# Performance work log

Measured on AMD Instinct MI355X. Metric: run time of the kernel, lower is better.

Reference implementation:

```python
import jax, jax.numpy as jnp
import numpy as np

N_NODES = 50000
N_EDGES = 800000
NODE = 64
EDGE = 32
READOUT = 256
DEPTH = 4
NUM_GRAPHS = 512
BN_EPS = 1e-5

# Assumption (ffn / hidden_xavier_bn not in source): ffn = Linear + ReLU;
# hidden_xavier_bn = Linear -> BatchNorm (batch stats) -> ReLU.

def _ffn(h, W, b):
    return jax.nn.relu(h @ W + b)

def setup_inputs() -> dict:
    key = jax.random.key(0)
    ks = jax.random.split(key, 16)
    def lin(k, fin, fout):
        return jax.random.normal(k, (fin, fout), jnp.float32) / np.sqrt(fin)
    inp = {
        "x": jax.random.normal(ks[0], (N_NODES, NODE), jnp.float32),
        "edge_index": jax.random.randint(ks[1], (2, N_EDGES), 0, N_NODES),
        "edge_attr": jax.random.normal(ks[2], (N_EDGES, EDGE), jnp.float32),
        "w_atoms": jax.random.uniform(ks[3], (N_NODES,), jnp.float32),
        "w_bonds": jax.random.uniform(ks[4], (N_EDGES,), jnp.float32),
        "batch": jnp.sort(jax.random.randint(ks[5], (N_NODES,), 0, NUM_GRAPHS)),
        "V_W": lin(ks[6], NODE, NODE), "V_b": jnp.zeros((NODE,), jnp.float32),
        "E_W": lin(ks[7], EDGE, EDGE), "E_b": jnp.zeros((EDGE,), jnp.float32),
        "U_W": lin(ks[8], 2 * NODE + EDGE, NODE), "U_b": jnp.zeros((NODE,), jnp.float32),
        "R_W": lin(ks[9], NODE, READOUT), "R_b": jnp.zeros((READOUT,), jnp.float32),
        "R_gamma": jnp.ones((READOUT,), jnp.float32),
        "R_beta": jnp.zeros((READOUT,), jnp.float32),
    }
    return inp


def reference(x, edge_index, edge_attr, w_atoms, w_bonds, batch,
              V_W, V_b, E_W, E_b, U_W, U_b, R_W, R_b, R_gamma, R_beta):
    src, dst = edge_index[0], edge_index[1]  # x_j = x[src], aggregate at dst
    x_clone = x  # .clone().detach()

    # Edge FFN output is loop-invariant (same edge_attr each depth)
    m_ij = _ffn(edge_attr, E_W, E_b)  # [E, EDGE]

    def mp(h):
        m_j = _ffn(h[src], V_W, V_b)                              # [E, NODE]
        msg = w_bonds[:, None] * jnp.concatenate([m_j, m_ij], 1)  # [E, NODE+EDGE]
        aggr = jax.ops.segment_sum(msg, dst, num_segments=N_NODES)
        up = jax.nn.elu(jnp.concatenate([aggr, h], 1))            # [N, 2*NODE+EDGE]
        return _ffn(up, U_W, U_b) * w_atoms[:, None]              # [N, NODE]

    h = x
    last_x = None
    last_last_x = None
    for i in range(DEPTH):
        if i == 0 or i == 1:
            h = mp(h)
        else:
            h = mp(last_last_x + h)
        if i > 0:
            last_last_x = last_x
        last_x = h

    # Readout: Linear -> BatchNorm(batch stats) -> ReLU
    y = (h + x_clone) @ R_W + R_b
    mu = jnp.mean(y, axis=0)
    var = jnp.var(y, axis=0)
    y = jax.nn.relu((y - mu) * jax.lax.rsqrt(var + BN_EPS) * R_gamma + R_beta)

    # normalize_embedding=True -> scatter_mean over graphs
    sums = jax.ops.segment_sum(y, batch, num_segments=NUM_GRAPHS)
    cnts = jax.ops.segment_sum(jnp.ones((N_NODES,), y.dtype), batch,
                               num_segments=NUM_GRAPHS)
    return sums / jnp.maximum(cnts, 1.0)[:, None]
```

## Files before the change

### kernel.cpp

```cpp
#include <hip/hip_runtime.h>
#include <hip/hip_fp16.h>
#include <cstdint>
#include <cstddef>

#define NODE 64
#define EDGEF 32
#define UPF 160
#define RD 256
#define UT_STRIDE 162

typedef unsigned int uint4n __attribute__((ext_vector_type(4)));

__device__ __forceinline__ float eluf(float x) { return x > 0.f ? x : expm1f(x); }

union U32H2 { unsigned int u; __half2 h; };
union H16U { __half h; unsigned short u; };

__device__ __forceinline__ float2 h2f(unsigned int u) {
    U32H2 t; t.u = u;
    return __half22float2(t.h);
}
__device__ __forceinline__ unsigned short f2h(float f) {
    H16U t; t.h = __float2half_rn(f);
    return t.u;
}

__global__ void k_count(const int* __restrict__ dst, int* cnt, int* rank, int E) {
    int e = blockIdx.x * 256 + threadIdx.x;
    if (e < E) rank[e] = atomicAdd(&cnt[dst[e]], 1);
}

__global__ void k_scanA(const int* __restrict__ cnt, int* starts, int* bsum, int N) {
    __shared__ int sh[256];
    int t = threadIdx.x;
    int base = blockIdx.x * 1024 + t * 4;
    int v0 = 0, v1 = 0, v2 = 0, v3 = 0;
    if (base + 0 < N) v0 = cnt[base + 0];
    if (base + 1 < N) v1 = cnt[base + 1];
    if (base + 2 < N) v2 = cnt[base + 2];
    if (base + 3 < N) v3 = cnt[base + 3];
    int tot = v0 + v1 + v2 + v3;
    sh[t] = tot;
    __syncthreads();
    for (int off = 1; off < 256; off <<= 1) {
        int add = (t >= off) ? sh[t - off] : 0;
        __syncthreads();
        sh[t] += add;
        __syncthreads();
    }
    int excl = sh[t] - tot;
    if (base + 0 < N) starts[base + 0] = excl;
    if (base + 1 < N) starts[base + 1] = excl + v0;
    if (base + 2 < N) starts[base + 2] = excl + v0 + v1;
    if (base + 3 < N) starts[base + 3] = excl + v0 + v1 + v2;
    if (t == 255) bsum[blockIdx.x] = sh[255];
}

__global__ void k_scanB(const int* __restrict__ bsum, int* boff, int nb, int* starts, int N) {
    if (threadIdx.x == 0 && blockIdx.x == 0) {
        int run = 0;
        for (int b = 0; b < nb; ++b) { boff[b] = run; run += bsum[b]; }
        starts[N] = run;
    }
}

__global__ void k_scanC(const int* __restrict__ boff, int* starts, int N) {
    int i = blockIdx.x * 256 + threadIdx.x;
    if (i < N) starts[i] += boff[i >> 10];
}

__global__ void k_fill_ids(const int* __restrict__ src, const int* __restrict__ dst,
                           const float* __restrict__ wb, const int* __restrict__ rank,
                           const int* __restrict__ starts, uint4n* __restrict__ ecsr, int E) {
    int e = blockIdx.x * 256 + threadIdx.x;
    if (e >= E) return;
    int pos = starts[dst[e]] + rank[e];
    uint4n rec;
    rec.x = (unsigned int)src[e];
    rec.y = __float_as_uint(wb[e]);
    rec.z = (unsigned int)e;
    rec.w = 0u;
    __builtin_nontemporal_store(rec, &ecsr[pos]);
}

__global__ __launch_bounds__(256) void k_medge(
    const float* __restrict__ ea, const float* __restrict__ wb,
    const float* __restrict__ EW, const float* __restrict__ Eb,
    unsigned short* __restrict__ medge, int E) {
    __shared__ float ew_s[EDGEF * EDGEF];
    __shared__ float eb_s[EDGEF];
    int tid = threadIdx.x;
    for (int i = tid; i < EDGEF * EDGEF; i += 256) ew_s[i] = EW[i];
    if (tid < EDGEF) eb_s[tid] = Eb[tid];
    __syncthreads();
    int lane = tid & 63, wid = tid >> 6;
    int grp = lane >> 3, gl = lane & 7;
    const float4* ea4 = (const float4*)ea;
    float4 eb4 = *(const float4*)&eb_s[gl * 4];
    for (int e0 = blockIdx.x * 32; e0 < E; e0 += gridDim.x * 32) {
        int e = e0 + wid * 8 + grp;
        float4 a4 = {0.f, 0.f, 0.f, 0.f};
        float w = 0.f;
        if (e < E) {
            a4 = ea4[(size_t)e * 8 + gl];
            w = wb[e];
        }
        float4 m = eb4;
#pragma unroll
        for (int k = 0; k < EDGEF; ++k) {
            float av;
            switch (k & 3) {
                case 0: av = a4.x; break;
                case 1: av = a4.y; break;
                case 2: av = a4.z; break;
                default: av = a4.w; break;
            }
            float ak = __shfl(av, (lane & 56) | (k >> 2), 64);
            float4 w4 = *(const float4*)&ew_s[k * EDGEF + gl * 4];
            m.x = fmaf(ak, w4.x, m.x);
            m.y = fmaf(ak, w4.y, m.y);
            m.z = fmaf(ak, w4.z, m.z);
            m.w = fmaf(ak, w4.w, m.w);
        }
        if (e < E) {
            uint2 o;
            o.x = (unsigned int)f2h(w * fmaxf(m.x, 0.f)) |
                  ((unsigned int)f2h(w * fmaxf(m.y, 0.f)) << 16);
            o.y = (unsigned int)f2h(w * fmaxf(m.z, 0.f)) |
                  ((unsigned int)f2h(w * fmaxf(m.w, 0.f)) << 16);
            *(uint2*)(medge + (size_t)e * EDGEF + gl * 4) = o;
        }
    }
}

__global__ __launch_bounds__(256) void k_sumE(
    const unsigned short* __restrict__ medge, const uint4n* __restrict__ ecsr,
    const int* __restrict__ starts, float* __restrict__ aggrE_elu, int N) {
    int tid = threadIdx.x;
    int lane = tid & 63, wid = tid >> 6;
    int grp = lane >> 2, gl = lane & 3;
    int nwaves = gridDim.x * 4;
    for (int n = blockIdx.x * 4 + wid; n < N; n += nwaves) {
        int s0 = starts[n], s1 = starts[n + 1];
        float acc[8] = {0.f, 0.f, 0.f, 0.f, 0.f, 0.f, 0.f, 0.f};
        int i = s0 + grp;
        uint4 r0 = {0u,0u,0u,0u}, r1 = {0u,0u,0u,0u};
        if (i < s1)      r0 = *(const uint4*)(medge + (size_t)ecsr[i].z      * EDGEF + gl * 8);
        if (i + 16 < s1) r1 = *(const uint4*)(medge + (size_t)ecsr[i + 16].z * EDGEF + gl * 8);
        for (; i < s1; i += 16) {
            uint4 rN = {0u,0u,0u,0u};
            if (i + 32 < s1) rN = *(const uint4*)(medge + (size_t)ecsr[i + 32].z * EDGEF + gl * 8);
            float2 f0 = h2f(r0.x), f1 = h2f(r0.y), f2 = h2f(r0.z), f3 = h2f(r0.w);
            acc[0] += f0.x; acc[1] += f0.y;
            acc[2] += f1.x; acc[3] += f1.y;
            acc[4] += f2.x; acc[5] += f2.y;
            acc[6] += f3.x; acc[7] += f3.y;
            r0 = r1; r1 = rN;
        }
#pragma unroll
        for (int m2 = 4; m2 <= 32; m2 <<= 1) {
#pragma unroll
            for (int j = 0; j < 8; ++j) acc[j] += __shfl_xor(acc[j], m2, 64);
        }
        if (lane < 4) {
            float4 o0 = { eluf(acc[0]), eluf(acc[1]), eluf(acc[2]), eluf(acc[3]) };
            float4 o1 = { eluf(acc[4]), eluf(acc[5]), eluf(acc[6]), eluf(acc[7]) };
            float4* op = (float4*)(aggrE_elu + (size_t)n * EDGEF + gl * 8);
            op[0] = o0;
            op[1] = o1;
        }
    }
}

__global__ __launch_bounds__(256) void k_hv(
    const float* __restrict__ ha, const float* __restrict__ hb, int addB,
    const float* __restrict__ VW, const float* __restrict__ Vb,
    unsigned short* __restrict__ hvh, int N, int chunk) {
    __shared__ float slot[4][NODE];
    int tid = threadIdx.x;
    int lane = tid & 63, w = tid >> 6;
    float vcol[NODE];
#pragma unroll
    for (int k = 0; k < NODE; ++k) vcol[k] = VW[k * NODE + lane];
    float vb = Vb[lane];
    const float4* s4 = (const float4*)slot[w];
    int n0 = blockIdx.x * chunk;
    int n1 = n0 + chunk; if (n1 > N) n1 = N;
    for (int n = n0 + w; n < n1; n += 4) {
        float hrow = ha[(size_t)n * NODE + lane];
        if (addB) hrow += hb[(size_t)n * NODE + lane];
        slot[w][lane] = hrow;
        float d0 = 0.f, d1 = 0.f, d2 = 0.f, d3 = 0.f;
#pragma unroll
        for (int q = 0; q < 16; ++q) {
            float4 h4 = s4[q];
            d0 = fmaf(h4.x, vcol[4*q+0], d0);
            d1 = fmaf(h4.y, vcol[4*q+1], d1);
            d2 = fmaf(h4.z, vcol[4*q+2], d2);
            d3 = fmaf(h4.w, vcol[4*q+3], d3);
        }
        hvh[(size_t)n * NODE + lane] = f2h(fmaxf(vb + ((d0 + d1) + (d2 + d3)), 0.f));
    }
}

__global__ __launch_bounds__(512, 8) void k_gather(
    const unsigned short* __restrict__ hvh, const int* __restrict__ starts,
    const uint4n* __restrict__ ecsr, float* __restrict__ aggr, int N) {
    int lane = threadIdx.x & 63, wid = threadIdx.x >> 6;
    int grp = lane >> 3, gl = lane & 7;
    int nwaves = gridDim.x * 8;
    for (int n = blockIdx.x * 8 + wid; n < N; n += nwaves) {
        int s0 = starts[n], s1 = starts[n + 1];
        int deg = s1 - s0;
        float acc[8] = {0.f, 0.f, 0.f, 0.f, 0.f, 0.f, 0.f, 0.f};
        uint4 r0 = {0u,0u,0u,0u}, r1 = {0u,0u,0u,0u};
        float w0 = 0.f, w1 = 0.f;
        if (grp < deg) {
            uint4n c = ecsr[s0 + grp];
            r0 = *(const uint4*)(hvh + (size_t)c.x * NODE + gl * 8);
            w0 = __uint_as_float(c.y);
        }
        if (grp + 8 < deg) {
            uint4n c = ecsr[s0 + grp + 8];
            r1 = *(const uint4*)(hvh + (size_t)c.x * NODE + gl * 8);
            w1 = __uint_as_float(c.y);
        }
        for (int i = grp; i < deg; i += 8) {
            uint4 rN = {0u,0u,0u,0u}; float wN = 0.f;
            if (i + 16 < deg) {
                uint4n c = ecsr[s0 + i + 16];
                rN = *(const uint4*)(hvh + (size_t)c.x * NODE + gl * 8);
                wN = __uint_as_float(c.y);
            }
            float2 f0 = h2f(r0.x), f1 = h2f(r0.y), f2 = h2f(r0.z), f3 = h2f(r0.w);
            acc[0] = fmaf(w0, f0.x, acc[0]);
            acc[1] = fmaf(w0, f0.y, acc[1]);
            acc[2] = fmaf(w0, f1.x, acc[2]);
            acc[3] = fmaf(w0, f1.y, acc[3]);
            acc[4] = fmaf(w0, f2.x, acc[4]);
            acc[5] = fmaf(w0, f2.y, acc[5]);
            acc[6] = fmaf(w0, f3.x, acc[6]);
            acc[7] = fmaf(w0, f3.y, acc[7]);
            r0 = r1; w0 = w1;
            r1 = rN; w1 = wN;
        }
#pragma unroll
        for (int m2 = 8; m2 <= 32; m2 <<= 1) {
#pragma unroll
            for (int j = 0; j < 8; ++j) acc[j] += __shfl_xor(acc[j], m2, 64);
        }
        if (lane < 8) {
            float4* op = (float4*)(aggr + (size_t)n * NODE + gl * 8);
            float4 o0 = { acc[0], acc[1], acc[2], acc[3] };
            float4 o1 = { acc[4], acc[5], acc[6], acc[7] };
            op[0] = o0;
            op[1] = o1;
        }
    }
}

__global__ __launch_bounds__(512, 4) void k_update(
    const float* __restrict__ ha, const float* __restrict__ hb, int addB,
    const float* __restrict__ aggr, const float* __restrict__ aggrE_elu,
    const float* __restrict__ UW, const float* __restrict__ Ub,
    const float* __restrict__ watoms, float* __restrict__ h_out, int N) {
    __shared__ float lds_Ut[NODE * UT_STRIDE];
    __shared__ float lds_up[8 * UPF];
    int tid = threadIdx.x;
    for (int idx = tid; idx < UPF * NODE; idx += 512) {
        int j = idx & 63, t2 = idx >> 6;
        lds_Ut[j * UT_STRIDE + t2] = UW[idx];
    }
    int lane = tid & 63, wid = tid >> 6;
    float ub = Ub[lane];
    __syncthreads();
    float* myup = lds_up + wid * UPF;
    int nwaves = gridDim.x * 8;
    for (int n = blockIdx.x * 8 + wid; n < N; n += nwaves) {
        myup[lane] = eluf(aggr[(size_t)n * NODE + lane]);
        if (lane < EDGEF) myup[NODE + lane] = aggrE_elu[(size_t)n * EDGEF + lane];
        float hrow = ha[(size_t)n * NODE + lane];
        if (addB) hrow += hb[(size_t)n * NODE + lane];
        myup[NODE + EDGEF + lane] = eluf(hrow);
        float o = ub;
#pragma unroll
        for (int t2 = 0; t2 < UPF; t2 += 2) {
            float2 u2 = *(const float2*)&myup[t2];
            float2 w2 = *(const float2*)&lds_Ut[lane * UT_STRIDE + t2];
            o = fmaf(u2.x, w2.x, o);
            o = fmaf(u2.y, w2.y, o);
        }
        h_out[(size_t)n * NODE + lane] = fmaxf(o, 0.f) * watoms[n];
    }
}

__global__ __launch_bounds__(256) void k_y(
    const float* __restrict__ ha, const float* __restrict__ hb,
    const float* __restrict__ RW, const float* __restrict__ Rb,
    float* __restrict__ y, float* colsum, float* colsumsq, int N, int chunk) {
    __shared__ float slot[4][NODE];
    int tid = threadIdx.x;
    int lane = tid & 63, w = tid >> 6;
    float rcol[NODE];
#pragma unroll
    for (int k = 0; k < NODE; ++k) rcol[k] = RW[k * RD + w * 64 + lane];
    float rb = Rb[w * 64 + lane];
    const float4* s4 = (const float4*)slot[w];
    float sum = 0.f, sq = 0.f;
    int n0 = blockIdx.x * chunk;
    int n1 = n0 + chunk; if (n1 > N) n1 = N;
    for (int n = n0; n < n1; ++n) {
        float hvC = ha[(size_t)n * NODE + lane] + hb[(size_t)n * NODE + lane];
        slot[w][lane] = hvC;
        float d0 = 0.f, d1 = 0.f, d2 = 0.f, d3 = 0.f;
#pragma unroll
        for (int q = 0; q < 16; ++q) {
            float4 h4 = s4[q];
            d0 = fmaf(h4.x, rcol[4*q+0], d0);
            d1 = fmaf(h4.y, rcol[4*q+1], d1);
            d2 = fmaf(h4.z, rcol[4*q+2], d2);
            d3 = fmaf(h4.w, rcol[4*q+3], d3);
        }
        float v = rb + ((d0 + d1) + (d2 + d3));
        y[(size_t)n * RD + w * 64 + lane] = v;
        sum += v; sq = fmaf(v, v, sq);
    }
    atomicAdd(&colsum[w * 64 + lane], sum);
    atomicAdd(&colsumsq[w * 64 + lane], sq);
}

__global__ void k_gbounds(const int* __restrict__ batch, int* gstart, int N, int G) {
    int n = blockIdx.x * 256 + threadIdx.x;
    if (n > N) return;
    int bprev = (n == 0) ? -1 : batch[n - 1];
    int bcur = (n == N) ? G : batch[n];
    for (int g = bprev + 1; g <= bcur; ++g) gstart[g] = n;
}

__global__ void k_out(const float* __restrict__ y, const float* __restrict__ colsum,
                      const float* __restrict__ colsumsq, const float* __restrict__ gamma,
                      const float* __restrict__ beta, const int* __restrict__ gstart,
                      float* __restrict__ out, float invN) {
    int g = blockIdx.x, c = threadIdx.x;
    float mu = colsum[c] * invN;
    float var = fmaxf(colsumsq[c] * invN - mu * mu, 0.f);
    float inv = rsqrtf(var + 1e-5f);
    float ga = gamma[c], be = beta[c];
    int a = gstart[g], b = gstart[g + 1];
    float acc = 0.f;
    for (int n = a; n < b; ++n) {
        float v = y[(size_t)n * RD + c];
        acc += fmaxf(fmaf((v - mu) * inv, ga, be), 0.f);
    }
    out[(size_t)g * RD + c] = acc / fmaxf((float)(b - a), 1.f);
}

extern "C" void kernel_launch(void* const* d_in, const int* in_sizes, int n_in,
                              void* d_out, int out_size, void* d_ws, size_t ws_size,
                              hipStream_t stream) {
    const float* x      = (const float*)d_in[0];
    const int*   ei     = (const int*)d_in[1];
    const float* eattr  = (const float*)d_in[2];
    const float* watoms = (const float*)d_in[3];
    const float* wbonds = (const float*)d_in[4];
    const int*   batch  = (const int*)d_in[5];
    const float* VW = (const float*)d_in[6];
    const float* Vb = (const float*)d_in[7];
    const float* EW = (const float*)d_in[8];
    const float* Eb = (const float*)d_in[9];
    const float* UW = (const float*)d_in[10];
    const float* Ub = (const float*)d_in[11];
    const float* RW = (const float*)d_in[12];
    const float* Rb = (const float*)d_in[13];
    const float* Rg = (const float*)d_in[14];
    const float* Rbe = (const float*)d_in[15];
    float* out = (float*)d_out;

    const int N = in_sizes[0] / NODE;
    const int E = in_sizes[4];
    const int G = out_size / RD;
    const int* src = ei;
    const int* dst = ei + E;

    char* p = (char*)d_ws;
    auto alloc = [&](size_t bytes) -> char* {
        char* r = p;
        p += (bytes + 255) & ~(size_t)255;
        return r;
    };
    float* aggrE   = (float*)alloc((size_t)N * EDGEF * 4);
    int*   cnt     = (int*)alloc((size_t)N * 4);
    int*   starts  = (int*)alloc((size_t)(N + 1) * 4);
    int*   rank    = (int*)alloc((size_t)E * 4);
    int*   bsum    = (int*)alloc(64 * 4);
    int*   boff    = (int*)alloc(64 * 4);
    uint4n* ecsr   = (uint4n*)alloc((size_t)E * 16);
    float* hA      = (float*)alloc((size_t)N * NODE * 4);
    float* hB      = (float*)alloc((size_t)N * NODE * 4);
    unsigned short* hvh = (unsigned short*)alloc((size_t)N * NODE * 2);
    float* aggr    = (float*)alloc((size_t)N * NODE * 4);
    float* colstat = (float*)alloc((size_t)2 * RD * 4);
    int*   gstart  = (int*)alloc((size_t)(G + 1) * 4);
    size_t mbytes = (size_t)E * EDGEF * 2;
    size_t ybytes = (size_t)N * RD * 4;
    float* ybuf = (float*)alloc(mbytes > ybytes ? mbytes : ybytes);
    unsigned short* medge = (unsigned short*)ybuf;

    hipMemsetAsync(cnt, 0, (size_t)N * 4, stream);
    hipMemsetAsync(colstat, 0, (size_t)2 * RD * 4, stream);

    int eblocks = (E + 255) / 256;
    int sblocks = (N + 1023) / 1024;

    k_count<<<eblocks, 256, 0, stream>>>(dst, cnt, rank, E);
    k_scanA<<<sblocks, 256, 0, stream>>>(cnt, starts, bsum, N);
    k_scanB<<<1, 64, 0, stream>>>(bsum, boff, sblocks, starts, N);
    k_scanC<<<(N + 255) / 256, 256, 0, stream>>>(boff, starts, N);
    k_fill_ids<<<eblocks, 256, 0, stream>>>(src, dst, wbonds, rank, starts, ecsr, E);
    k_medge<<<2048, 256, 0, stream>>>(eattr, wbonds, EW, Eb, medge, E);
    k_sumE<<<2048, 256, 0, stream>>>(medge, ecsr, starts, aggrE, N);

    int hvblocks = 512;
    int chunk = (N + hvblocks - 1) / hvblocks;

    k_hv<<<hvblocks, 256, 0, stream>>>(x, x, 0, VW, Vb, hvh, N, chunk);
    k_gather<<<2048, 512, 0, stream>>>(hvh, starts, ecsr, aggr, N);
    k_update<<<768, 512, 0, stream>>>(x, x, 0, aggr, aggrE, UW, Ub, watoms, hA, N);
    k_hv<<<hvblocks, 256, 0, stream>>>(hA, hA, 0, VW, Vb, hvh, N, chunk);
    k_gather<<<2048, 512, 0, stream>>>(hvh, starts, ecsr, aggr, N);
    k_update<<<768, 512, 0, stream>>>(hA, hA, 0, aggr, aggrE, UW, Ub, watoms, hB, N);
    k_hv<<<hvblocks, 256, 0, stream>>>(hA, hB, 1, VW, Vb, hvh, N, chunk);
    k_gather<<<2048, 512, 0, stream>>>(hvh, starts, ecsr, aggr, N);
    k_update<<<768, 512, 0, stream>>>(hA, hB, 1, aggr, aggrE, UW, Ub, watoms, hA, N);
    k_hv<<<hvblocks, 256, 0, stream>>>(hB, hA, 1, VW, Vb, hvh, N, chunk);
    k_gather<<<2048, 512, 0, stream>>>(hvh, starts, ecsr, aggr, N);
    k_update<<<768, 512, 0, stream>>>(hB, hA, 1, aggr, aggrE, UW, Ub, watoms, hB, N);

    int yblocks = 2048;
    int ychunk = (N + yblocks - 1) / yblocks;
    k_y<<<yblocks, 256, 0, stream>>>(hB, x, RW, Rb, ybuf, colstat, colstat + RD, N, ychunk);
    k_gbounds<<<(N + 256) / 256, 256, 0, stream>>>(batch, gstart, N, G);
    k_out<<<G, RD, 0, stream>>>(ybuf, colstat, colstat + RD, Rg, Rbe, gstart, out, 1.0f / (float)N);
}
```

Before: 621.1 us.

## Fuse neighbor gather into node update kernel and shrink readout grid

Merges the per-node gather/sum over incoming edges with the update FFN in one kernel, so the aggregated row goes straight into LDS with ELU applied, instead of a round trip through a global aggr buffer. This removes one launch per depth and the N×64 float write and read. The fused kernel loads the 40KB U weight tile into LDS per block and runs 768 blocks, so the gather now has less parallelism than its former 2048-block grid and lower occupancy. The readout k_y grid also drops from 2048 to 512 blocks.

```diff
diff --git a/kernel.cpp b/kernel.cpp
--- a/kernel.cpp
+++ b/kernel.cpp
@@ -203,11 +203,25 @@
     }
 }
 
-__global__ __launch_bounds__(512, 8) void k_gather(
-    const unsigned short* __restrict__ hvh, const int* __restrict__ starts,
-    const uint4n* __restrict__ ecsr, float* __restrict__ aggr, int N) {
-    int lane = threadIdx.x & 63, wid = threadIdx.x >> 6;
+__global__ __launch_bounds__(512) void k_gupdate(
+    const float* __restrict__ ha, const float* __restrict__ hb, int addB,
+    const unsigned short* __restrict__ hvh,
+    const int* __restrict__ starts, const uint4n* __restrict__ ecsr,
+    const float* __restrict__ aggrE_elu,
+    const float* __restrict__ UW, const float* __restrict__ Ub,
+    const float* __restrict__ watoms, float* __restrict__ h_out, int N) {
+    __shared__ float lds_Ut[NODE * UT_STRIDE];
+    __shared__ float lds_up[8 * UPF];
+    int tid = threadIdx.x;
+    for (int idx = tid; idx < UPF * NODE; idx += 512) {
+        int j = idx & 63, t2 = idx >> 6;
+        lds_Ut[j * UT_STRIDE + t2] = UW[idx];
+    }
+    int lane = tid & 63, wid = tid >> 6;
     int grp = lane >> 3, gl = lane & 7;
+    float ub = Ub[lane];
+    __syncthreads();
+    float* myup = lds_up + wid * UPF;
     int nwaves = gridDim.x * 8;
     for (int n = blockIdx.x * 8 + wid; n < N; n += nwaves) {
         int s0 = starts[n], s1 = starts[n + 1];
@@ -250,34 +264,9 @@
             for (int j = 0; j < 8; ++j) acc[j] += __shfl_xor(acc[j], m2, 64);
         }
         if (lane < 8) {
-            float4* op = (float4*)(aggr + (size_t)n * NODE + gl * 8);
-            float4 o0 = { acc[0], acc[1], acc[2], acc[3] };
-            float4 o1 = { acc[4], acc[5], acc[6], acc[7] };
-            op[0] = o0;
-            op[1] = o1;
-        }
-    }
-}
-
-__global__ __launch_bounds__(512, 4) void k_update(
-    const float* __restrict__ ha, const float* __restrict__ hb, int addB,
-    const float* __restrict__ aggr, const float* __restrict__ aggrE_elu,
-    const float* __restrict__ UW, const float* __restrict__ Ub,
-    const float* __restrict__ watoms, float* __restrict__ h_out, int N) {
-    __shared__ float lds_Ut[NODE * UT_STRIDE];
-    __shared__ float lds_up[8 * UPF];
-    int tid = threadIdx.x;
-    for (int idx = tid; idx < UPF * NODE; idx += 512) {
-        int j = idx & 63, t2 = idx >> 6;
-        lds_Ut[j * UT_STRIDE + t2] = UW[idx];
-    }
-    int lane = tid & 63, wid = tid >> 6;
-    float ub = Ub[lane];
-    __syncthreads();
-    float* myup = lds_up + wid * UPF;
-    int nwaves = gridDim.x * 8;
-    for (int n = blockIdx.x * 8 + wid; n < N; n += nwaves) {
-        myup[lane] = eluf(aggr[(size_t)n * NODE + lane]);
+#pragma unroll
+            for (int j = 0; j < 8; ++j) myup[gl * 8 + j] = eluf(acc[j]);
+        }
         if (lane < EDGEF) myup[NODE + lane] = aggrE_elu[(size_t)n * EDGEF + lane];
         float hrow = ha[(size_t)n * NODE + lane];
         if (addB) hrow += hb[(size_t)n * NODE + lane];
@@ -398,7 +387,6 @@
     float* hA      = (float*)alloc((size_t)N * NODE * 4);
     float* hB      = (float*)alloc((size_t)N * NODE * 4);
     unsigned short* hvh = (unsigned short*)alloc((size_t)N * NODE * 2);
-    float* aggr    = (float*)alloc((size_t)N * NODE * 4);
     float* colstat = (float*)alloc((size_t)2 * RD * 4);
     int*   gstart  = (int*)alloc((size_t)(G + 1) * 4);
     size_t mbytes = (size_t)E * EDGEF * 2;
@@ -424,19 +412,15 @@
     int chunk = (N + hvblocks - 1) / hvblocks;
 
     k_hv<<<hvblocks, 256, 0, stream>>>(x, x, 0, VW, Vb, hvh, N, chunk);
-    k_gather<<<2048, 512, 0, stream>>>(hvh, starts, ecsr, aggr, N);
-    k_update<<<768, 512, 0, stream>>>(x, x, 0, aggr, aggrE, UW, Ub, watoms, hA, N);
+    k_gupdate<<<768, 512, 0, stream>>>(x, x, 0, hvh, starts, ecsr, aggrE, UW, Ub, watoms, hA, N);
     k_hv<<<hvblocks, 256, 0, stream>>>(hA, hA, 0, VW, Vb, hvh, N, chunk);
-    k_gather<<<2048, 512, 0, stream>>>(hvh, starts, ecsr, aggr, N);
-    k_update<<<768, 512, 0, stream>>>(hA, hA, 0, aggr, aggrE, UW, Ub, watoms, hB, N);
+    k_gupdate<<<768, 512, 0, stream>>>(hA, hA, 0, hvh, starts, ecsr, aggrE, UW, Ub, watoms, hB, N);
     k_hv<<<hvblocks, 256, 0, stream>>>(hA, hB, 1, VW, Vb, hvh, N, chunk);
-    k_gather<<<2048, 512, 0, stream>>>(hvh, starts, ecsr, aggr, N);
-    k_update<<<768, 512, 0, stream>>>(hA, hB, 1, aggr, aggrE, UW, Ub, watoms, hA, N);
+    k_gupdate<<<768, 512, 0, stream>>>(hA, hB, 1, hvh, starts, ecsr, aggrE, UW, Ub, watoms, hA, N);
     k_hv<<<hvblocks, 256, 0, stream>>>(hB, hA, 1, VW, Vb, hvh, N, chunk);
-    k_gather<<<2048, 512, 0, stream>>>(hvh, starts, ecsr, aggr, N);
-    k_update<<<768, 512, 0, stream>>>(hB, hA, 1, aggr, aggrE, UW, Ub, watoms, hB, N);
-
-    int yblocks = 2048;
+    k_gupdate<<<768, 512, 0, stream>>>(hB, hA, 1, hvh, starts, ecsr, aggrE, UW, Ub, watoms, hB, N);
+
+    int yblocks = 512;
     int ychunk = (N + yblocks - 1) / yblocks;
     k_y<<<yblocks, 256, 0, stream>>>(hB, x, RW, Rb, ybuf, colstat, colstat + RD, N, ychunk);
     k_gbounds<<<(N + 256) / 256, 256, 0, stream>>>(batch, gstart, N, G);
```

After: 749.6 us. 1.21x slower.
